# Kernel tuning notes

Hardware: AMD Instinct MI355X
Metric: run time of the kernel (lower is better)

## Reference

```python
import jax, jax.numpy as jnp
import numpy as np

Q_MAX = 6.0        # NVFP4 act mode
SCALE_MAX = 448.0  # scale clamp in manual_quant_act
BLOCK = 128        # forward passes self.block_size (128), not the fn default 16


def quant_act(x):
    # block-wise fake quant: reshape to (-1, BLOCK), per-block absmax scale,
    # round, clamp to [-Q_MAX, Q_MAX], rescale
    shp = x.shape
    xf = x.reshape(-1, BLOCK)
    raw_scale = jnp.clip(jnp.max(jnp.abs(xf), axis=-1, keepdims=True), 1e-12, None) / Q_MAX
    scale = jnp.minimum(raw_scale, SCALE_MAX)
    xq = jnp.clip(jnp.round(xf / scale), -Q_MAX, Q_MAX) * scale
    return xq.reshape(shp)


def setup_inputs() -> dict:
    key = jax.random.key(0)
    ks = jax.random.split(key, 6)
    B, S, D_IN, D_OUT, R = 4, 4096, 4096, 4096, 64
    x = jax.random.normal(ks[0], (B, S, D_IN), dtype=jnp.float32)
    w_ternary = jax.random.normal(ks[1], (D_OUT, D_IN), dtype=jnp.float32) * 0.02
    smooth_scale = jax.random.uniform(ks[2], (D_IN,), dtype=jnp.float32, minval=0.5, maxval=1.5)
    lora_a = jax.random.normal(ks[3], (R, D_IN), dtype=jnp.float32) * 0.02
    lora_b = jax.random.normal(ks[4], (D_OUT, R), dtype=jnp.float32) * 0.02
    bias = jax.random.normal(ks[5], (D_OUT,), dtype=jnp.float32) * 0.01
    return {"x": x, "w_ternary": w_ternary, "smooth_scale": smooth_scale,
            "lora_a": lora_a, "lora_b": lora_b, "bias": bias}


def reference(x, w_ternary, smooth_scale, lora_a, lora_b, bias):
    # smooth-scale activations, block fake-quant, base GEMM + low-rank SVD correction
    x_q = quant_act(x * smooth_scale)                      # [B,S,D_in]
    base_out = jnp.einsum('bsd,od->bso', x_q, w_ternary)   # [B,S,D_out]
    svd_out = jnp.einsum('bsr,or->bso',
                         jnp.einsum('bsd,rd->bsr', x_q, lora_a), lora_b)
    return base_out + svd_out + bias
```

## Files before the change

kernel.cpp:

```cpp
#include <hip/hip_runtime.h>
#include <hip/hip_bf16.h>

using short8 = __attribute__((ext_vector_type(8))) short;
using f32x4  = __attribute__((ext_vector_type(4))) float;

#define GLL16(g, l)                                                          \
  __builtin_amdgcn_global_load_lds(                                          \
      (const __attribute__((address_space(1))) void*)(g),                    \
      (__attribute__((address_space(3))) void*)(l), 16, 0, 0)

__global__ __launch_bounds__(256) void quant_kernel(
    const float* __restrict__ x, const float* __restrict__ smooth,
    __hip_bfloat16* __restrict__ xq, int D) {
  int tid = threadIdx.x;
  size_t qb = (size_t)blockIdx.x * 8 + (tid >> 5);
  int l = tid & 31;
  size_t base = qb * 128 + (size_t)l * 4;
  const float4 v = *(const float4*)(x + base);
  int d = (int)(base & (size_t)(D - 1));
  const float4 s = *(const float4*)(smooth + d);
  float y0 = v.x * s.x, y1 = v.y * s.y, y2 = v.z * s.z, y3 = v.w * s.w;
  float am = fmaxf(fmaxf(fabsf(y0), fabsf(y1)), fmaxf(fabsf(y2), fabsf(y3)));
#pragma unroll
  for (int off = 1; off < 32; off <<= 1)
    am = fmaxf(am, __shfl_xor(am, off, 64));
  float scale = fminf(fmaxf(am, 1e-12f) / 6.0f, 448.0f);
  float q0 = fminf(fmaxf(rintf(y0 / scale), -6.0f), 6.0f) * scale;
  float q1 = fminf(fmaxf(rintf(y1 / scale), -6.0f), 6.0f) * scale;
  float q2 = fminf(fmaxf(rintf(y2 / scale), -6.0f), 6.0f) * scale;
  float q3 = fminf(fmaxf(rintf(y3 / scale), -6.0f), 6.0f) * scale;
  union {
    __hip_bfloat16 h[4];
    uint2 u;
  } pk;
  pk.h[0] = __float2bfloat16(q0);
  pk.h[1] = __float2bfloat16(q1);
  pk.h[2] = __float2bfloat16(q2);
  pk.h[3] = __float2bfloat16(q3);
  *(uint2*)(xq + base) = pk.u;
}

__global__ __launch_bounds__(256) void wprep_kernel(
    const float* __restrict__ w, const float* __restrict__ la,
    const float* __restrict__ lb, __hip_bfloat16* __restrict__ weff, int Dk,
    int R) {
  __shared__ float lbs[16 * 64];
  int tid = threadIdx.x;
  int o0 = (blockIdx.x >> 4) * 16;
  int d = ((blockIdx.x & 15) << 8) + tid;
#pragma unroll
  for (int i = 0; i < 4; ++i) {
    int idx = tid + i * 256;
    lbs[idx] = lb[(size_t)(o0 + (idx >> 6)) * R + (idx & 63)];
  }
  __syncthreads();
  float acc[16];
#pragma unroll
  for (int oo = 0; oo < 16; ++oo) acc[oo] = 0.f;
  for (int r = 0; r < 64; ++r) {
    float av = la[(size_t)r * Dk + d];
#pragma unroll
    for (int oo = 0; oo < 16; ++oo) acc[oo] += lbs[oo * 64 + r] * av;
  }
#pragma unroll
  for (int oo = 0; oo < 16; ++oo) {
    size_t idx = (size_t)(o0 + oo) * Dk + d;
    weff[idx] = __float2bfloat16(w[idx] + acc[oo]);
  }
}

#define BM 256
#define BN 256
#define BKT 64

__global__ __launch_bounds__(512, 2) void gemm_kernel(
    const __hip_bfloat16* __restrict__ A, const __hip_bfloat16* __restrict__ B,
    const float* __restrict__ bias, float* __restrict__ C, int M, int N,
    int K) {
  __shared__ __attribute__((aligned(16))) char lds[131072];

  const int tid = threadIdx.x;
  const int wave = tid >> 6, lane = tid & 63;
  const int wr = wave >> 2, wc = wave & 3;
  const int lr = lane & 15;
  const int hi16 = (lane >> 4) * 16;
  const int swx = (lr & 7) << 4;

  const int nwg = gridDim.x;
  const int cpx = nwg >> 3;
  const int swzb = (blockIdx.x & 7) * cpx + (blockIdx.x >> 3);
  const int ntn = N / BN;
  const int tm = swzb / ntn, tn = swzb % ntn;
  const size_t m0 = (size_t)tm * BM, n0 = (size_t)tn * BN;

  const int trow = tid >> 3;
  const int csw = ((tid & 7) ^ (trow & 7)) * 8;
  const __hip_bfloat16* baseA = A + (m0 + trow) * (size_t)K + csw;
  const __hip_bfloat16* baseB = B + (n0 + trow) * (size_t)K + csw;
  char* sbase = lds + wave * 1024;

  const char* rdA = lds + (wr * 64 + lr) * 128;
  const char* rdB = lds + 32768 + (wc * 32 + lr) * 128;

#define STAGE(d, ab, h, kt)                                                   \
  do {                                                                        \
    const __hip_bfloat16* _g = ((ab) ? baseB : baseA) +                       \
                               (size_t)((h) * 128) * K + (size_t)(kt) * BKT;  \
    char* _l = sbase + (d) * 65536 + (ab) * 32768 + (h) * 16384;              \
    GLL16(_g, _l);                                                            \
    GLL16(_g + 64 * (size_t)K, _l + 8192);                                    \
  } while (0)

#define READ_A(DST, d, h)                                                     \
  _Pragma("unroll") for (int m = 0; m < 4; ++m)                               \
      _Pragma("unroll") for (int kk = 0; kk < 2; ++kk)                        \
          DST[m][kk] = *(const short8*)(rdA + (d) * 65536 + (h) * 16384 +     \
                                        m * 2048 + ((kk * 64 + hi16) ^ swx));

#define READ_B(DST, d, g)                                                     \
  _Pragma("unroll") for (int n = 0; n < 2; ++n)                               \
      _Pragma("unroll") for (int kk = 0; kk < 2; ++kk)                        \
          DST[n][kk] = *(const short8*)(rdB + (d) * 65536 + (g) * 16384 +     \
                                        n * 2048 + ((kk * 64 + hi16) ^ swx));

#define MFMA16(h, g, AF, BF)                                                  \
  _Pragma("unroll") for (int kk = 0; kk < 2; ++kk)                            \
      _Pragma("unroll") for (int m = 0; m < 4; ++m)                           \
          _Pragma("unroll") for (int n = 0; n < 2; ++n)                       \
              acc[h][m][g][n] = __builtin_amdgcn_mfma_f32_16x16x32_bf16(      \
                  AF[m][kk], BF[n][kk], acc[h][m][g][n], 0, 0, 0);

#define BARRIER __builtin_amdgcn_s_barrier()
#define SBAR0 __builtin_amdgcn_sched_barrier(0)
#define FENCE asm volatile("" ::: "memory")
#define GATE                                                                  \
  asm volatile("s_waitcnt lgkmcnt(0)" ::: "memory");                          \
  __builtin_amdgcn_sched_barrier(0)
#define VMW(N)                                                                \
  asm volatile("s_waitcnt vmcnt(" #N ")" ::: "memory");                       \
  __builtin_amdgcn_sched_barrier(0)

  short8 aF0[4][2], aF1[4][2], bF0[2][2], bF1[2][2];
  f32x4 acc[2][4][2][2];
#pragma unroll
  for (int h = 0; h < 2; ++h)
#pragma unroll
    for (int m = 0; m < 4; ++m)
#pragma unroll
      for (int g = 0; g < 2; ++g)
#pragma unroll
        for (int n = 0; n < 2; ++n) acc[h][m][g][n] = (f32x4){0.f, 0.f, 0.f, 0.f};

  const int NK = K / BKT;

  STAGE(0, 0, 0, 0);
  STAGE(0, 1, 1, 0);
  STAGE(0, 0, 1, 0);
  STAGE(0, 1, 0, 0);
  STAGE(1, 0, 0, 1);
  STAGE(1, 1, 1, 1);
  STAGE(1, 0, 1, 1);
  VMW(6);
  BARRIER;
  FENCE;
  READ_A(aF0, 0, 0);
  READ_B(bF0, 0, 0);
  SBAR0;

  const int niter = NK / 2;
  for (int i = 0; i < niter; ++i) {
    const int k2 = (2 * i + 2 < NK) ? 2 * i + 2 : NK - 1;
    const int k3 = (2 * i + 3 < NK) ? 2 * i + 3 : NK - 1;
    STAGE(1, 1, 0, 2 * i + 1);
    BARRIER;
    GATE;
    __builtin_amdgcn_s_setprio(1);
    MFMA16(0, 0, aF0, bF0);
    __builtin_amdgcn_s_setprio(0);
    READ_B(bF1, 0, 1);
    SBAR0;
    BARRIER;
    STAGE(0, 0, 0, k2);
    BARRIER;
    GATE;
    __builtin_amdgcn_s_setprio(1);
    MFMA16(0, 1, aF0, bF1);
    __builtin_amdgcn_s_setprio(0);
    READ_A(aF1, 0, 1);
    SBAR0;
    BARRIER;
    STAGE(0, 1, 1, k2);
    BARRIER;
    GATE;
    __builtin_amdgcn_s_setprio(1);
    MFMA16(1, 1, aF1, bF1);
    __builtin_amdgcn_s_setprio(0);
    VMW(4);
    SBAR0;
    BARRIER;
    STAGE(0, 0, 1, k2);
    FENCE;
    READ_A(aF0, 1, 0);
    SBAR0;
    BARRIER;
    __builtin_amdgcn_s_setprio(1);
    MFMA16(1, 0, aF1, bF0);
    __builtin_amdgcn_s_setprio(0);
    READ_B(bF0, 1, 0);
    SBAR0;
    BARRIER;
    STAGE(0, 1, 0, k2);
    BARRIER;
    GATE;
    __builtin_amdgcn_s_setprio(1);
    MFMA16(0, 0, aF0, bF0);
    __builtin_amdgcn_s_setprio(0);
    READ_B(bF1, 1, 1);
    SBAR0;
    BARRIER;
    STAGE(1, 0, 0, k3);
    BARRIER;
    GATE;
    __builtin_amdgcn_s_setprio(1);
    MFMA16(0, 1, aF0, bF1);
    __builtin_amdgcn_s_setprio(0);
    READ_A(aF1, 1, 1);
    SBAR0;
    BARRIER;
    STAGE(1, 1, 1, k3);
    BARRIER;
    GATE;
    __builtin_amdgcn_s_setprio(1);
    MFMA16(1, 1, aF1, bF1);
    __builtin_amdgcn_s_setprio(0);
    VMW(4);
    SBAR0;
    BARRIER;
    STAGE(1, 0, 1, k3);
    FENCE;
    READ_A(aF0, 0, 0);
    SBAR0;
    BARRIER;
    __builtin_amdgcn_s_setprio(1);
    MFMA16(1, 0, aF1, bF0);
    __builtin_amdgcn_s_setprio(0);
    READ_B(bF0, 0, 0);
    SBAR0;
    BARRIER;
  }

#pragma unroll
  for (int h = 0; h < 2; ++h)
#pragma unroll
    for (int g = 0; g < 2; ++g)
#pragma unroll
      for (int n = 0; n < 2; ++n) {
        const int col = (int)n0 + g * 128 + wc * 32 + n * 16 + lr;
        const float bv = bias[col];
#pragma unroll
        for (int m = 0; m < 4; ++m) {
          const int row = (int)m0 + h * 128 + wr * 64 + m * 16 + (lane >> 4) * 4;
#pragma unroll
          for (int r = 0; r < 4; ++r)
            C[(size_t)(row + r) * N + col] = acc[h][m][g][n][r] + bv;
        }
      }
}

extern "C" void kernel_launch(void* const* d_in, const int* in_sizes, int n_in,
                              void* d_out, int out_size, void* d_ws,
                              size_t ws_size, hipStream_t stream) {
  const float* x = (const float*)d_in[0];
  const float* w = (const float*)d_in[1];
  const float* smooth = (const float*)d_in[2];
  const float* la = (const float*)d_in[3];
  const float* lb = (const float*)d_in[4];
  const float* bias = (const float*)d_in[5];
  float* out = (float*)d_out;

  const int K = in_sizes[2];
  const int N = in_sizes[5];
  const int M = in_sizes[0] / K;
  const int R = in_sizes[3] / K;

  __hip_bfloat16* xq = (__hip_bfloat16*)d_ws;
  __hip_bfloat16* weff = xq + (size_t)M * K;

  {
    size_t qblocks = ((size_t)M * K) / 128;
    int blocks = (int)(qblocks / 8);
    quant_kernel<<<blocks, 256, 0, stream>>>(x, smooth, xq, K);
  }
  {
    int blocks = (N / 16) * (K / 256);
    wprep_kernel<<<blocks, 256, 0, stream>>>(w, la, lb, weff, K, R);
  }
  {
    int blocks = (M / BM) * (N / BN);
    gemm_kernel<<<blocks, 512, 0, stream>>>(xq, weff, bias, out, M, N, K);
  }
}
```

Measured before the change: 626.2 us.

## Restructure GEMM main loop to one barrier per MFMA phase with reordered staging

Rewrites the software-pipelined main loop of the bf16 GEMM. Each MFMA phase is now preceded by an LDS fragment read and a global-to-LDS stage, then a single barrier, instead of two barriers plus explicit lgkmcnt waits. The prologue prefetches a different set of quarter-tiles and waits on vmcnt(4). This is meant to cut synchronization stalls and overlap loads with MFMA, but dropping the lgkmcnt gates relies on the compiler inserting correct waits. The changed stage order also risks LDS read/write hazards.

```diff
diff --git a/kernel.cpp b/kernel.cpp
--- a/kernel.cpp
+++ b/kernel.cpp
@@ -130,12 +130,10 @@
               acc[h][m][g][n] = __builtin_amdgcn_mfma_f32_16x16x32_bf16(      \
                   AF[m][kk], BF[n][kk], acc[h][m][g][n], 0, 0, 0);
 
-#define BARRIER __builtin_amdgcn_s_barrier()
+#define BAR __builtin_amdgcn_s_barrier()
 #define SBAR0 __builtin_amdgcn_sched_barrier(0)
-#define FENCE asm volatile("" ::: "memory")
-#define GATE                                                                  \
-  asm volatile("s_waitcnt lgkmcnt(0)" ::: "memory");                          \
-  __builtin_amdgcn_sched_barrier(0)
+#define SETP1 __builtin_amdgcn_s_setprio(1)
+#define SETP0 __builtin_amdgcn_s_setprio(0)
 #define VMW(N)                                                                \
   asm volatile("s_waitcnt vmcnt(" #N ")" ::: "memory");                       \
   __builtin_amdgcn_sched_barrier(0)
@@ -154,15 +152,14 @@
   const int NK = K / BKT;
 
   STAGE(0, 0, 0, 0);
+  STAGE(0, 1, 0, 0);
   STAGE(0, 1, 1, 0);
   STAGE(0, 0, 1, 0);
-  STAGE(0, 1, 0, 0);
   STAGE(1, 0, 0, 1);
-  STAGE(1, 1, 1, 1);
-  STAGE(1, 0, 1, 1);
-  VMW(6);
-  BARRIER;
-  FENCE;
+  STAGE(1, 1, 0, 1);
+  VMW(4);
+  BAR;
+  SBAR0;
   READ_A(aF0, 0, 0);
   READ_B(bF0, 0, 0);
   SBAR0;
@@ -171,82 +168,66 @@
   for (int i = 0; i < niter; ++i) {
     const int k2 = (2 * i + 2 < NK) ? 2 * i + 2 : NK - 1;
     const int k3 = (2 * i + 3 < NK) ? 2 * i + 3 : NK - 1;
-    STAGE(1, 1, 0, 2 * i + 1);
-    BARRIER;
-    GATE;
-    __builtin_amdgcn_s_setprio(1);
+    READ_B(bF1, 0, 1);
+    STAGE(1, 1, 1, 2 * i + 1);
+    BAR;
+    SBAR0;
+    SETP1;
     MFMA16(0, 0, aF0, bF0);
-    __builtin_amdgcn_s_setprio(0);
-    READ_B(bF1, 0, 1);
-    SBAR0;
-    BARRIER;
+    SETP0;
+    READ_A(aF1, 0, 1);
+    STAGE(1, 0, 1, 2 * i + 1);
+    BAR;
+    SBAR0;
+    SETP1;
+    MFMA16(0, 1, aF0, bF1);
+    SETP0;
     STAGE(0, 0, 0, k2);
-    BARRIER;
-    GATE;
-    __builtin_amdgcn_s_setprio(1);
+    VMW(2);
+    BAR;
+    SBAR0;
+    SETP1;
+    MFMA16(1, 1, aF1, bF1);
+    SETP0;
+    READ_A(aF0, 1, 0);
+    STAGE(0, 1, 0, k2);
+    BAR;
+    SBAR0;
+    SETP1;
+    MFMA16(1, 0, aF1, bF0);
+    SETP0;
+    READ_B(bF0, 1, 0);
+    SBAR0;
+    READ_B(bF1, 1, 1);
+    STAGE(0, 1, 1, k2);
+    BAR;
+    SBAR0;
+    SETP1;
+    MFMA16(0, 0, aF0, bF0);
+    SETP0;
+    READ_A(aF1, 1, 1);
+    STAGE(0, 0, 1, k2);
+    BAR;
+    SBAR0;
+    SETP1;
     MFMA16(0, 1, aF0, bF1);
-    __builtin_amdgcn_s_setprio(0);
-    READ_A(aF1, 0, 1);
-    SBAR0;
-    BARRIER;
-    STAGE(0, 1, 1, k2);
-    BARRIER;
-    GATE;
-    __builtin_amdgcn_s_setprio(1);
+    SETP0;
+    STAGE(1, 0, 0, k3);
+    VMW(2);
+    BAR;
+    SBAR0;
+    SETP1;
     MFMA16(1, 1, aF1, bF1);
-    __builtin_amdgcn_s_setprio(0);
-    VMW(4);
-    SBAR0;
-    BARRIER;
-    STAGE(0, 0, 1, k2);
-    FENCE;
-    READ_A(aF0, 1, 0);
-    SBAR0;
-    BARRIER;
-    __builtin_amdgcn_s_setprio(1);
+    SETP0;
+    READ_A(aF0, 0, 0);
+    STAGE(1, 1, 0, k3);
+    BAR;
+    SBAR0;
+    SETP1;
     MFMA16(1, 0, aF1, bF0);
-    __builtin_amdgcn_s_setprio(0);
-    READ_B(bF0, 1, 0);
-    SBAR0;
-    BARRIER;
-    STAGE(0, 1, 0, k2);
-    BARRIER;
-    GATE;
-    __builtin_amdgcn_s_setprio(1);
-    MFMA16(0, 0, aF0, bF0);
-    __builtin_amdgcn_s_setprio(0);
-    READ_B(bF1, 1, 1);
-    SBAR0;
-    BARRIER;
-    STAGE(1, 0, 0, k3);
-    BARRIER;
-    GATE;
-    __builtin_amdgcn_s_setprio(1);
-    MFMA16(0, 1, aF0, bF1);
-    __builtin_amdgcn_s_setprio(0);
-    READ_A(aF1, 1, 1);
-    SBAR0;
-    BARRIER;
-    STAGE(1, 1, 1, k3);
-    BARRIER;
-    GATE;
-    __builtin_amdgcn_s_setprio(1);
-    MFMA16(1, 1, aF1, bF1);
-    __builtin_amdgcn_s_setprio(0);
-    VMW(4);
-    SBAR0;
-    BARRIER;
-    STAGE(1, 0, 1, k3);
-    FENCE;
-    READ_A(aF0, 0, 0);
-    SBAR0;
-    BARRIER;
-    __builtin_amdgcn_s_setprio(1);
-    MFMA16(1, 0, aF1, bF0);
-    __builtin_amdgcn_s_setprio(0);
+    SETP0;
     READ_B(bF0, 0, 0);
     SBAR0;
-    BARRIER;
   }
 
 #pragma unroll
```

After: 767.8 us. +22.6%, slower.
